# Optimization experiments

Measured on AMD Instinct MI355X. Metric: run time of the kernel, lower is better.

## Reference

```python
import jax, jax.numpy as jnp
import numpy as np

B, S, H = 2, 2048, 1024          # batch, seq, hidden_size
I = 512                          # expert_ffn_hidden_size
E_R, E_Z = 32, 8                 # routed experts, zero (identity) experts
E_T = E_R + E_Z                  # total experts
K = 6                            # moe_topk
SCALE = 2.5                      # routed_scaling_factor
W_INIT = 0.02


def setup_inputs() -> dict:
    key = jax.random.key(0)
    k0, k1, k2, k3 = jax.random.split(key, 4)
    return {
        "hidden_states": jax.random.normal(k0, (B, S, H), jnp.float32),
        "classifier_weight": jax.random.normal(k1, (E_T, H), jnp.float32) * W_INIT,
        "e_score_correction_bias": jnp.zeros((E_T,), jnp.float32),
        "gate_up_proj": jax.random.normal(k2, (E_T, 2 * I, H), jnp.float32) * W_INIT,
        "down_proj": jax.random.normal(k3, (E_R, H, I), jnp.float32) * W_INIT,
    }


def reference(hidden_states, classifier_weight, e_score_correction_bias,
              gate_up_proj, down_proj):
    orig_shape = hidden_states.shape
    x = hidden_states.reshape(-1, H).astype(jnp.float32)      # [T, H]
    T = x.shape[0]

    # ---- router (fp32 like the torch code) ----
    logits = x @ classifier_weight.T                          # [T, E_T]
    scores = jax.nn.softmax(logits, axis=-1)
    _, topk_idx = jax.lax.top_k(scores + e_score_correction_bias[None, :], K)
    topk_w = jnp.take_along_axis(scores, topk_idx, axis=1) * SCALE  # [T, K]

    # dense per-(token, expert) combine weights; 0 for unselected experts
    w_full = jnp.zeros((T, E_T), jnp.float32).at[
        jnp.arange(T)[:, None], topk_idx].add(topk_w)          # [T, E_T]

    # zero experts: weighted identity
    zero_w = w_full[:, E_R:].sum(axis=-1, keepdims=True)       # [T, 1]
    out0 = x * zero_w

    # routed experts: SwiGLU MLP per expert, scanned over experts
    routed_w = w_full[:, :E_R].T                               # [E_R, T]

    def body(out, xs):
        Wgu, Wd, we = xs                                       # [2I,H],[H,I],[T]
        gate, up = jnp.split(x @ Wgu.T, 2, axis=-1)            # [T, I] each
        y = (jax.nn.silu(gate) * up) @ Wd.T                    # [T, H]
        return out + we[:, None] * y, None

    out, _ = jax.lax.scan(body, out0, (gate_up_proj[:E_R], down_proj, routed_w))
    return out.reshape(orig_shape).astype(hidden_states.dtype)
```

## Files before the change

### kernel.cpp

```cpp
#include <hip/hip_runtime.h>
#include <float.h>
#include <math.h>

#define TT 4096
#define HH 1024
#define II 512
#define E_R 32
#define E_T 40
#define TOPK 6
#define SCALE_F 2.5f
#define MAXTILES 224

typedef __bf16 bf16x8 __attribute__((ext_vector_type(8)));
typedef float f32x4 __attribute__((ext_vector_type(4)));

__device__ inline unsigned short f2bf(float f) {
  __bf16 h = (__bf16)f;
  return __builtin_bit_cast(unsigned short, h);
}

__device__ inline bf16x8 cvt8v(float4 a, float4 b) {
  bf16x8 v;
  v[0] = (__bf16)a.x; v[1] = (__bf16)a.y; v[2] = (__bf16)a.z; v[3] = (__bf16)a.w;
  v[4] = (__bf16)b.x; v[5] = (__bf16)b.y; v[6] = (__bf16)b.z; v[7] = (__bf16)b.w;
  return v;
}

__device__ inline void gload_lds16(const void* g, void* l) {
  __builtin_amdgcn_global_load_lds(
      (__attribute__((address_space(1))) void*)g,
      (__attribute__((address_space(3))) void*)l, 16, 0, 0);
}

__device__ inline bf16x8 lds_frag(const unsigned short* base, int row, int kb) {
  int byte = (row * 128 + kb * 2) ^ ((row & 7) << 4);
  uint4 v = *reinterpret_cast<const uint4*>(reinterpret_cast<const char*>(base) + byte);
  return __builtin_bit_cast(bf16x8, v);
}

__device__ inline bf16x8 lds_frag_f32(const float* base, int row, int kb) {
  int key = row & 15;
  int c0 = (kb >> 2) ^ key;
  int c1 = ((kb >> 2) + 1) ^ key;
  const char* p = reinterpret_cast<const char*>(base) + row * 256;
  float4 lo = *reinterpret_cast<const float4*>(p + c0 * 16);
  float4 hi = *reinterpret_cast<const float4*>(p + c1 * 16);
  return cvt8v(lo, hi);
}

__device__ inline f32x4 mfma16(bf16x8 a, bf16x8 b, f32x4 c) {
  return __builtin_amdgcn_mfma_f32_16x16x32_bf16(a, b, c, 0, 0, 0);
}

__global__ __launch_bounds__(256) void k_logits(const float* __restrict__ x,
                                                const float* __restrict__ wcls,
                                                float* __restrict__ logits,
                                                unsigned short* __restrict__ xb,
                                                int* __restrict__ counts) {
  __shared__ float4 ws4[E_T * 64];
  const int tid = threadIdx.x;
  const int lane = tid & 63;
  const int wave = tid >> 6;
  const int token = blockIdx.x * 4 + wave;
  if (blockIdx.x == 0 && tid < E_R) counts[tid] = 0;
  const float4* x4 = reinterpret_cast<const float4*>(x);
  const float4* w4 = reinterpret_cast<const float4*>(wcls);

  float acc[E_T];
  #pragma unroll
  for (int e = 0; e < E_T; ++e) acc[e] = 0.f;

  for (int c = 0; c < 4; ++c) {
    if (c) __syncthreads();
    #pragma unroll
    for (int j = 0; j < 10; ++j) {
      int v = tid + j * 256;
      int e = v >> 6, kq = v & 63;
      ws4[v] = w4[e * 256 + c * 64 + kq];
    }
    float4 xv = x4[(size_t)token * 256 + c * 64 + lane];
    ushort4 s;
    s.x = f2bf(xv.x); s.y = f2bf(xv.y); s.z = f2bf(xv.z); s.w = f2bf(xv.w);
    reinterpret_cast<ushort4*>(xb + (size_t)token * HH)[c * 64 + lane] = s;
    __syncthreads();
    #pragma unroll
    for (int e = 0; e < E_T; ++e) {
      float4 w = ws4[e * 64 + lane];
      acc[e] += xv.x * w.x + xv.y * w.y + xv.z * w.z + xv.w * w.w;
    }
  }

  float mine = 0.f;
  #pragma unroll
  for (int e = 0; e < E_T; ++e) {
    float r = acc[e];
    #pragma unroll
    for (int o = 32; o; o >>= 1) r += __shfl_xor(r, o);
    if (lane == e) mine = r;
  }
  if (lane < E_T) logits[(size_t)token * E_T + lane] = mine;
}

__global__ void k_topk(const float* __restrict__ logits, const float* __restrict__ bias,
                       float* __restrict__ zero_w, int* __restrict__ counts,
                       int* __restrict__ tok_list,
                       int* __restrict__ route_ep, float* __restrict__ route_w,
                       int* __restrict__ route_n) {
  int t = blockIdx.x * 64 + threadIdx.x;
  float l[E_T];
  const float4* lp = reinterpret_cast<const float4*>(logits + (size_t)t * E_T);
  #pragma unroll
  for (int j = 0; j < E_T / 4; ++j) {
    float4 v = lp[j];
    l[j * 4 + 0] = v.x; l[j * 4 + 1] = v.y; l[j * 4 + 2] = v.z; l[j * 4 + 3] = v.w;
  }
  float m = -FLT_MAX;
  #pragma unroll
  for (int e = 0; e < E_T; ++e) m = fmaxf(m, l[e]);
  float den = 0.f;
  #pragma unroll
  for (int e = 0; e < E_T; ++e) { l[e] = __expf(l[e] - m); den += l[e]; }
  float inv = 1.f / den;
  float sel[E_T];
  #pragma unroll
  for (int e = 0; e < E_T; ++e) { l[e] *= inv; sel[e] = l[e] + bias[e]; }

  unsigned long long used = 0ull;
  float zw = 0.f;
  int nr = 0;
  for (int k = 0; k < TOPK; ++k) {
    float bv = -FLT_MAX; int bj = 0;
    #pragma unroll
    for (int e = 0; e < E_T; ++e) {
      float v = ((used >> e) & 1ull) ? -FLT_MAX : sel[e];
      if (v > bv) { bv = v; bj = e; }
    }
    used |= 1ull << bj;
    float wgt = (bv - bias[bj]) * SCALE_F;
    if (bj >= E_R) {
      zw += wgt;
    } else {
      int p = atomicAdd(&counts[bj], 1);
      tok_list[bj * TT + p] = t;
      route_ep[t * TOPK + nr] = (bj << 16) | p;
      route_w[t * TOPK + nr] = wgt;
      nr++;
    }
  }
  zero_w[t] = zw;
  route_n[t] = nr;
}

__global__ void k_scan(const int* __restrict__ counts, int* __restrict__ offsets,
                       int* __restrict__ tiles) {
  if (threadIdx.x == 0) {
    int s = 0, idx = 0;
    for (int e = 0; e < E_R; ++e) {
      offsets[e] = s;
      int c = counts[e];
      s += c;
      for (int r0 = 0; r0 < c; r0 += 128) tiles[1 + idx++] = (e << 16) | r0;
    }
    offsets[E_R] = s;
    tiles[0] = idx;
  }
}

__global__ __launch_bounds__(256, 3) void k_gemm1(
    const unsigned short* __restrict__ xb, const float* __restrict__ gup,
    const int* __restrict__ tok_list, const int* __restrict__ counts,
    const int* __restrict__ offsets, const int* __restrict__ tiles,
    unsigned short* __restrict__ inter) {
  const int nt = tiles[0];
  if ((int)blockIdx.y >= nt) return;
  const int tv = tiles[1 + blockIdx.y];
  const int e = tv >> 16;
  const int row0 = tv & 0xffff;
  const int cnt = counts[e];
  const int off = offsets[e];
  const int n0 = blockIdx.x * 64;
  const int tid = threadIdx.x;
  const int lane = tid & 63;
  const int wave = tid >> 6;
  const int wr = wave >> 1;
  const int wc = wave & 1;

  __shared__ __align__(16) unsigned short lA[128 * 64];
  __shared__ __align__(16) float lBg[64 * 64];
  __shared__ __align__(16) float lBu[64 * 64];
  __shared__ int toks[128];

  if (tid < 128) {
    int r = row0 + tid;
    toks[tid] = tok_list[e * TT + (r < cnt ? r : cnt - 1)];
  }
  __syncthreads();

  unsigned aoff[4];
  #pragma unroll
  for (int i = 0; i < 4; ++i) {
    int lrow = wave * 32 + i * 8 + (lane >> 3);
    aoff[i] = (unsigned)toks[lrow] * HH + (((lane & 7) ^ (lrow & 7)) * 8);
  }
  const float* gbase = gup + (size_t)e * 1024 * HH;
  unsigned boff[4];
  #pragma unroll
  for (int i = 0; i < 4; ++i) {
    int rt = wave * 16 + i * 4 + (lane >> 4);
    boff[i] = (unsigned)(n0 + rt) * HH + (((lane & 15) ^ (rt & 15)) * 4);
  }
  const unsigned upjump = 512u * HH;

  f32x4 accg[4][2] = {}; f32x4 accu[4][2] = {};

  for (int k0 = 0; k0 < HH; k0 += 64) {
    #pragma unroll
    for (int i = 0; i < 4; ++i)
      gload_lds16(xb + aoff[i] + k0, lA + (wave * 32 + i * 8) * 64);
    #pragma unroll
    for (int i = 0; i < 4; ++i) {
      gload_lds16(gbase + boff[i] + k0,          lBg + (wave * 16 + i * 4) * 64);
      gload_lds16(gbase + boff[i] + upjump + k0, lBu + (wave * 16 + i * 4) * 64);
    }
    __syncthreads();
    #pragma unroll
    for (int ks = 0; ks < 2; ++ks) {
      int kb = ks * 32 + ((lane >> 4) << 3);
      bf16x8 a[4], g[2], u[2];
      #pragma unroll
      for (int i = 0; i < 4; ++i) a[i] = lds_frag(lA, wr * 64 + i * 16 + (lane & 15), kb);
      #pragma unroll
      for (int j = 0; j < 2; ++j) {
        g[j] = lds_frag_f32(lBg, wc * 32 + j * 16 + (lane & 15), kb);
        u[j] = lds_frag_f32(lBu, wc * 32 + j * 16 + (lane & 15), kb);
      }
      #pragma unroll
      for (int i = 0; i < 4; ++i)
        #pragma unroll
        for (int j = 0; j < 2; ++j) {
          accg[i][j] = mfma16(a[i], g[j], accg[i][j]);
          accu[i][j] = mfma16(a[i], u[j], accu[i][j]);
        }
    }
    __syncthreads();
  }

  #pragma unroll
  for (int i = 0; i < 4; ++i)
    #pragma unroll
    for (int j = 0; j < 2; ++j)
      #pragma unroll
      for (int r = 0; r < 4; ++r) {
        int rloc = wr * 64 + i * 16 + ((lane >> 4) << 2) + r;
        int grow = row0 + rloc;
        if (grow < cnt) {
          int col = n0 + wc * 32 + j * 16 + (lane & 15);
          float gv = accg[i][j][r], uv = accu[i][j][r];
          float act = gv / (1.f + __expf(-gv)) * uv;
          inter[(size_t)(off + grow) * II + col] = f2bf(act);
        }
      }
}

__global__ __launch_bounds__(256, 3) void k_gemm2(
    const unsigned short* __restrict__ inter, const float* __restrict__ dwn,
    const int* __restrict__ counts, const int* __restrict__ offsets,
    const int* __restrict__ tiles, unsigned short* __restrict__ inter2) {
  const int nt = tiles[0];
  if ((int)blockIdx.y >= nt) return;
  const int tv = tiles[1 + blockIdx.y];
  const int e = tv >> 16;
  const int row0 = tv & 0xffff;
  const int cnt = counts[e];
  const int off = offsets[e];
  const int h0 = blockIdx.x * 128;
  const int tid = threadIdx.x;
  const int lane = tid & 63;
  const int wave = tid >> 6;
  const int wr = wave >> 1;
  const int wc = wave & 1;

  __shared__ __align__(16) unsigned short lA[128 * 64];
  __shared__ __align__(16) float lB[128 * 64];

  unsigned aoff[4];
  #pragma unroll
  for (int i = 0; i < 4; ++i) {
    int lrow = wave * 32 + i * 8 + (lane >> 3);
    int rr = row0 + lrow; rr = rr < cnt ? rr : cnt - 1;
    aoff[i] = (unsigned)(off + rr) * II + (((lane & 7) ^ (lrow & 7)) * 8);
  }
  const float* dbase = dwn + (size_t)e * HH * II;
  unsigned boff[8];
  #pragma unroll
  for (int i = 0; i < 8; ++i) {
    int rt = wave * 32 + i * 4 + (lane >> 4);
    boff[i] = (unsigned)(h0 + rt) * II + (((lane & 15) ^ (rt & 15)) * 4);
  }

  f32x4 acc[4][4] = {};

  for (int k0 = 0; k0 < II; k0 += 64) {
    #pragma unroll
    for (int i = 0; i < 4; ++i)
      gload_lds16(inter + aoff[i] + k0, lA + (wave * 32 + i * 8) * 64);
    #pragma unroll
    for (int i = 0; i < 8; ++i)
      gload_lds16(dbase + boff[i] + k0, lB + (wave * 32 + i * 4) * 64);
    __syncthreads();
    #pragma unroll
    for (int ks = 0; ks < 2; ++ks) {
      int kb = ks * 32 + ((lane >> 4) << 3);
      bf16x8 a[4], b[4];
      #pragma unroll
      for (int i = 0; i < 4; ++i) a[i] = lds_frag(lA, wr * 64 + i * 16 + (lane & 15), kb);
      #pragma unroll
      for (int j = 0; j < 4; ++j) b[j] = lds_frag_f32(lB, wc * 64 + j * 16 + (lane & 15), kb);
      #pragma unroll
      for (int i = 0; i < 4; ++i)
        #pragma unroll
        for (int j = 0; j < 4; ++j)
          acc[i][j] = mfma16(a[i], b[j], acc[i][j]);
    }
    __syncthreads();
  }

  #pragma unroll
  for (int i = 0; i < 4; ++i)
    #pragma unroll
    for (int j = 0; j < 4; ++j)
      #pragma unroll
      for (int r = 0; r < 4; ++r) {
        int rloc = wr * 64 + i * 16 + ((lane >> 4) << 2) + r;
        int grow = row0 + rloc;
        if (grow < cnt) {
          int h = h0 + wc * 64 + j * 16 + (lane & 15);
          inter2[(size_t)(off + grow) * HH + h] = f2bf(acc[i][j][r]);
        }
      }
}

__global__ __launch_bounds__(256) void k_combine(
    const float* __restrict__ x, const float* __restrict__ zero_w,
    const int* __restrict__ offsets, const int* __restrict__ route_ep,
    const float* __restrict__ route_w, const int* __restrict__ route_n,
    const unsigned short* __restrict__ inter2, float* __restrict__ out) {
  const int t = blockIdx.x;
  const int tid = threadIdx.x;
  const float zw = zero_w[t];
  const int n = route_n[t];
  float4 o = reinterpret_cast<const float4*>(x)[t * 256 + tid];
  o.x *= zw; o.y *= zw; o.z *= zw; o.w *= zw;
  for (int i = 0; i < n; ++i) {
    int ep = route_ep[t * TOPK + i];
    int row = offsets[ep >> 16] + (ep & 0xffff);
    float w = route_w[t * TOPK + i];
    ushort4 v = reinterpret_cast<const ushort4*>(inter2 + (size_t)row * HH)[tid];
    o.x += w * __builtin_bit_cast(float, (unsigned)v.x << 16);
    o.y += w * __builtin_bit_cast(float, (unsigned)v.y << 16);
    o.z += w * __builtin_bit_cast(float, (unsigned)v.z << 16);
    o.w += w * __builtin_bit_cast(float, (unsigned)v.w << 16);
  }
  reinterpret_cast<float4*>(out)[t * 256 + tid] = o;
}


extern "C" void kernel_launch(void* const* d_in, const int* in_sizes, int n_in,
                              void* d_out, int out_size, void* d_ws, size_t ws_size,
                              hipStream_t stream) {
  const float* x    = (const float*)d_in[0];
  const float* wcls = (const float*)d_in[1];
  const float* bias = (const float*)d_in[2];
  const float* gup  = (const float*)d_in[3];
  const float* dwn  = (const float*)d_in[4];
  float* out = (float*)d_out;

  char* w = (char*)d_ws;
  unsigned short* xb    = (unsigned short*)(w + 0);
  float* zero_w         = (float*)(w + 8388608);
  int* counts           = (int*)(w + 8404992);
  int* offsets          = (int*)(w + 8405120);
  int* tok_list         = (int*)(w + 8405376);
  float* logits         = (float*)(w + 8929664);
  int* tiles            = (int*)(w + 9585024);
  int* route_ep         = (int*)(w + 9589120);
  float* route_w        = (float*)(w + 9687424);
  int* route_n          = (int*)(w + 9785728);
  unsigned short* inter = (unsigned short*)(w + 9802112);
  unsigned short* inter2 = (unsigned short*)(w + 34967936);

  k_logits<<<1024, 256, 0, stream>>>(x, wcls, logits, xb, counts);
  k_topk<<<64, 64, 0, stream>>>(logits, bias, zero_w, counts, tok_list,
                                route_ep, route_w, route_n);
  k_scan<<<1, 64, 0, stream>>>(counts, offsets, tiles);
  k_gemm1<<<dim3(8, MAXTILES), 256, 0, stream>>>(xb, gup, tok_list, counts, offsets, tiles, inter);
  k_gemm2<<<dim3(8, MAXTILES), 256, 0, stream>>>(inter, dwn, counts, offsets, tiles, inter2);
  k_combine<<<TT, 256, 0, stream>>>(x, zero_w, offsets, route_ep, route_w, route_n,
                                    inter2, out);
}
```

Before: 222.6 us.

## Pre-convert down_proj to bf16 and double-buffer gemm2 LDS loads

```diff
diff --git a/kernel.cpp b/kernel.cpp
--- a/kernel.cpp
+++ b/kernel.cpp
@@ -10,6 +10,7 @@
 #define TOPK 6
 #define SCALE_F 2.5f
 #define MAXTILES 224
+#define NDWN (32*1024*512)
 
 typedef __bf16 bf16x8 __attribute__((ext_vector_type(8)));
 typedef float f32x4 __attribute__((ext_vector_type(4)));
@@ -50,6 +51,19 @@
 
 __device__ inline f32x4 mfma16(bf16x8 a, bf16x8 b, f32x4 c) {
   return __builtin_amdgcn_mfma_f32_16x16x32_bf16(a, b, c, 0, 0, 0);
+}
+
+#define WAIT_VM8()  do { asm volatile("s_waitcnt vmcnt(8)" ::: "memory"); } while (0)
+#define WAIT_VM0()  do { asm volatile("s_waitcnt vmcnt(0)" ::: "memory"); } while (0)
+#define SBAR()      __builtin_amdgcn_s_barrier()
+#define SCHED0()    __builtin_amdgcn_sched_barrier(0)
+
+__global__ __launch_bounds__(256) void k_convert_dwn(const float* __restrict__ dwn,
+                                                     uint4* __restrict__ wb) {
+  unsigned i = blockIdx.x * 256 + threadIdx.x;
+  const float4* src = reinterpret_cast<const float4*>(dwn) + (size_t)i * 2;
+  float4 a = src[0], b = src[1];
+  wb[i] = __builtin_bit_cast(uint4, cvt8v(a, b));
 }
 
 __global__ __launch_bounds__(256) void k_logits(const float* __restrict__ x,
@@ -263,7 +277,7 @@
 }
 
 __global__ __launch_bounds__(256, 3) void k_gemm2(
-    const unsigned short* __restrict__ inter, const float* __restrict__ dwn,
+    const unsigned short* __restrict__ inter, const unsigned short* __restrict__ dwnb,
     const int* __restrict__ counts, const int* __restrict__ offsets,
     const int* __restrict__ tiles, unsigned short* __restrict__ inter2) {
   const int nt = tiles[0];
@@ -280,8 +294,8 @@
   const int wr = wave >> 1;
   const int wc = wave & 1;
 
-  __shared__ __align__(16) unsigned short lA[128 * 64];
-  __shared__ __align__(16) float lB[128 * 64];
+  __shared__ __align__(16) unsigned short lA[2][128 * 64];
+  __shared__ __align__(16) unsigned short lB[2][128 * 64];
 
   unsigned aoff[4];
   #pragma unroll
@@ -290,40 +304,65 @@
     int rr = row0 + lrow; rr = rr < cnt ? rr : cnt - 1;
     aoff[i] = (unsigned)(off + rr) * II + (((lane & 7) ^ (lrow & 7)) * 8);
   }
-  const float* dbase = dwn + (size_t)e * HH * II;
-  unsigned boff[8];
-  #pragma unroll
-  for (int i = 0; i < 8; ++i) {
-    int rt = wave * 32 + i * 4 + (lane >> 4);
-    boff[i] = (unsigned)(h0 + rt) * II + (((lane & 15) ^ (rt & 15)) * 4);
+  const unsigned short* db = dwnb + (size_t)e * (HH * II);
+  unsigned boff[4];
+  #pragma unroll
+  for (int i = 0; i < 4; ++i) {
+    int lrow = wave * 32 + i * 8 + (lane >> 3);
+    boff[i] = (unsigned)(h0 + lrow) * II + (((lane & 7) ^ (lrow & 7)) * 8);
   }
 
   f32x4 acc[4][4] = {};
 
-  for (int k0 = 0; k0 < II; k0 += 64) {
-    #pragma unroll
-    for (int i = 0; i < 4; ++i)
-      gload_lds16(inter + aoff[i] + k0, lA + (wave * 32 + i * 8) * 64);
-    #pragma unroll
-    for (int i = 0; i < 8; ++i)
-      gload_lds16(dbase + boff[i] + k0, lB + (wave * 32 + i * 4) * 64);
-    __syncthreads();
-    #pragma unroll
-    for (int ks = 0; ks < 2; ++ks) {
-      int kb = ks * 32 + ((lane >> 4) << 3);
-      bf16x8 a[4], b[4];
-      #pragma unroll
-      for (int i = 0; i < 4; ++i) a[i] = lds_frag(lA, wr * 64 + i * 16 + (lane & 15), kb);
-      #pragma unroll
-      for (int j = 0; j < 4; ++j) b[j] = lds_frag_f32(lB, wc * 64 + j * 16 + (lane & 15), kb);
-      #pragma unroll
-      for (int i = 0; i < 4; ++i)
-        #pragma unroll
-        for (int j = 0; j < 4; ++j)
-          acc[i][j] = mfma16(a[i], b[j], acc[i][j]);
-    }
-    __syncthreads();
-  }
+#define G2_STAGE(T, B)                                                          \
+  {                                                                             \
+    int k0s = (T) * 64;                                                         \
+    _Pragma("unroll")                                                           \
+    for (int i = 0; i < 4; ++i)                                                 \
+      gload_lds16(inter + aoff[i] + k0s, lA[B] + (wave * 32 + i * 8) * 64);     \
+    _Pragma("unroll")                                                           \
+    for (int i = 0; i < 4; ++i)                                                 \
+      gload_lds16(db + boff[i] + k0s, lB[B] + (wave * 32 + i * 8) * 64);        \
+  }
+
+#define G2_COMPUTE(B)                                                           \
+  {                                                                             \
+    _Pragma("unroll")                                                           \
+    for (int ks = 0; ks < 2; ++ks) {                                            \
+      int kb = ks * 32 + ((lane >> 4) << 3);                                    \
+      bf16x8 a[4], b[4];                                                        \
+      _Pragma("unroll")                                                         \
+      for (int i = 0; i < 4; ++i) a[i] = lds_frag(lA[B], wr * 64 + i * 16 + (lane & 15), kb); \
+      _Pragma("unroll")                                                         \
+      for (int j = 0; j < 4; ++j) b[j] = lds_frag(lB[B], wc * 64 + j * 16 + (lane & 15), kb); \
+      _Pragma("unroll")                                                         \
+      for (int i = 0; i < 4; ++i)                                               \
+        _Pragma("unroll")                                                       \
+        for (int j = 0; j < 4; ++j)                                             \
+          acc[i][j] = mfma16(a[i], b[j], acc[i][j]);                            \
+    }                                                                           \
+  }
+
+  G2_STAGE(0, 0);
+  G2_STAGE(1, 1);
+  WAIT_VM8();
+  SBAR(); SCHED0();
+
+  #pragma unroll 2
+  for (int t = 0; t < 6; ++t) {
+    if (t & 1) { G2_COMPUTE(1); } else { G2_COMPUTE(0); }
+    SCHED0();
+    SBAR();
+    if (t & 1) { G2_STAGE(t + 2, 1); } else { G2_STAGE(t + 2, 0); }
+    WAIT_VM8();
+    SBAR(); SCHED0();
+  }
+  G2_COMPUTE(0);
+  SCHED0();
+  SBAR();
+  WAIT_VM0();
+  SBAR(); SCHED0();
+  G2_COMPUTE(1);
 
   #pragma unroll
   for (int i = 0; i < 4; ++i)
@@ -388,13 +427,15 @@
   int* route_n          = (int*)(w + 9785728);
   unsigned short* inter = (unsigned short*)(w + 9802112);
   unsigned short* inter2 = (unsigned short*)(w + 34967936);
-
+  unsigned short* dwnb  = (unsigned short*)(w + 85299584);
+
+  k_convert_dwn<<<NDWN / 8 / 256, 256, 0, stream>>>(dwn, (uint4*)dwnb);
   k_logits<<<1024, 256, 0, stream>>>(x, wcls, logits, xb, counts);
   k_topk<<<64, 64, 0, stream>>>(logits, bias, zero_w, counts, tok_list,
                                 route_ep, route_w, route_n);
   k_scan<<<1, 64, 0, stream>>>(counts, offsets, tiles);
   k_gemm1<<<dim3(8, MAXTILES), 256, 0, stream>>>(xb, gup, tok_list, counts, offsets, tiles, inter);
-  k_gemm2<<<dim3(8, MAXTILES), 256, 0, stream>>>(inter, dwn, counts, offsets, tiles, inter2);
+  k_gemm2<<<dim3(8, MAXTILES), 256, 0, stream>>>(inter, dwnb, counts, offsets, tiles, inter2);
   k_combine<<<TT, 256, 0, stream>>>(x, zero_w, offsets, route_ep, route_w, route_n,
                                     inter2, out);
 }
```

After: 236.9 us. +6.4%, slower.

## Fold scan into topk via last-block ticket and remap GEMM grid for XCD locality

Applied to the files above, without the earlier changes.

```diff
diff --git a/kernel.cpp b/kernel.cpp
--- a/kernel.cpp
+++ b/kernel.cpp
@@ -56,13 +56,17 @@
                                                 const float* __restrict__ wcls,
                                                 float* __restrict__ logits,
                                                 unsigned short* __restrict__ xb,
-                                                int* __restrict__ counts) {
+                                                int* __restrict__ counts,
+                                                int* __restrict__ ticket) {
   __shared__ float4 ws4[E_T * 64];
   const int tid = threadIdx.x;
   const int lane = tid & 63;
   const int wave = tid >> 6;
   const int token = blockIdx.x * 4 + wave;
-  if (blockIdx.x == 0 && tid < E_R) counts[tid] = 0;
+  if (blockIdx.x == 0) {
+    if (tid < E_R) counts[tid] = 0;
+    else if (tid == E_R) *ticket = 0;
+  }
   const float4* x4 = reinterpret_cast<const float4*>(x);
   const float4* w4 = reinterpret_cast<const float4*>(wcls);
 
@@ -105,7 +109,9 @@
                        float* __restrict__ zero_w, int* __restrict__ counts,
                        int* __restrict__ tok_list,
                        int* __restrict__ route_ep, float* __restrict__ route_w,
-                       int* __restrict__ route_n) {
+                       int* __restrict__ route_n,
+                       int* __restrict__ offsets, int* __restrict__ tiles,
+                       int* __restrict__ ticket) {
   int t = blockIdx.x * 64 + threadIdx.x;
   float l[E_T];
   const float4* lp = reinterpret_cast<const float4*>(logits + (size_t)t * E_T);
@@ -149,20 +155,22 @@
   }
   zero_w[t] = zw;
   route_n[t] = nr;
-}
-
-__global__ void k_scan(const int* __restrict__ counts, int* __restrict__ offsets,
-                       int* __restrict__ tiles) {
+
+  __threadfence();
+  __syncthreads();
   if (threadIdx.x == 0) {
-    int s = 0, idx = 0;
-    for (int e = 0; e < E_R; ++e) {
-      offsets[e] = s;
-      int c = counts[e];
-      s += c;
-      for (int r0 = 0; r0 < c; r0 += 128) tiles[1 + idx++] = (e << 16) | r0;
-    }
-    offsets[E_R] = s;
-    tiles[0] = idx;
+    int tk = atomicAdd(ticket, 1);
+    if (tk == (int)gridDim.x - 1) {
+      int s = 0, idx = 0;
+      for (int e = 0; e < E_R; ++e) {
+        int c = atomicAdd(&counts[e], 0);
+        offsets[e] = s;
+        s += c;
+        for (int r0 = 0; r0 < c; r0 += 128) tiles[1 + idx++] = (e << 16) | r0;
+      }
+      offsets[E_R] = s;
+      tiles[0] = idx;
+    }
   }
 }
 
@@ -171,14 +179,17 @@
     const int* __restrict__ tok_list, const int* __restrict__ counts,
     const int* __restrict__ offsets, const int* __restrict__ tiles,
     unsigned short* __restrict__ inter) {
+  const int fid = blockIdx.x;
+  const int w = (fid & 7) * MAXTILES + (fid >> 3);
+  const int ty = w >> 3;
   const int nt = tiles[0];
-  if ((int)blockIdx.y >= nt) return;
-  const int tv = tiles[1 + blockIdx.y];
+  if (ty >= nt) return;
+  const int tv = tiles[1 + ty];
   const int e = tv >> 16;
   const int row0 = tv & 0xffff;
   const int cnt = counts[e];
   const int off = offsets[e];
-  const int n0 = blockIdx.x * 64;
+  const int n0 = (w & 7) * 64;
   const int tid = threadIdx.x;
   const int lane = tid & 63;
   const int wave = tid >> 6;
@@ -266,14 +277,17 @@
     const unsigned short* __restrict__ inter, const float* __restrict__ dwn,
     const int* __restrict__ counts, const int* __restrict__ offsets,
     const int* __restrict__ tiles, unsigned short* __restrict__ inter2) {
+  const int fid = blockIdx.x;
+  const int w = (fid & 7) * MAXTILES + (fid >> 3);
+  const int ty = w >> 3;
   const int nt = tiles[0];
-  if ((int)blockIdx.y >= nt) return;
-  const int tv = tiles[1 + blockIdx.y];
+  if (ty >= nt) return;
+  const int tv = tiles[1 + ty];
   const int e = tv >> 16;
   const int row0 = tv & 0xffff;
   const int cnt = counts[e];
   const int off = offsets[e];
-  const int h0 = blockIdx.x * 128;
+  const int h0 = (w & 7) * 128;
   const int tid = threadIdx.x;
   const int lane = tid & 63;
   const int wave = tid >> 6;
@@ -380,6 +394,7 @@
   float* zero_w         = (float*)(w + 8388608);
   int* counts           = (int*)(w + 8404992);
   int* offsets          = (int*)(w + 8405120);
+  int* ticket           = (int*)(w + 8405120 + 160);
   int* tok_list         = (int*)(w + 8405376);
   float* logits         = (float*)(w + 8929664);
   int* tiles            = (int*)(w + 9585024);
@@ -389,12 +404,11 @@
   unsigned short* inter = (unsigned short*)(w + 9802112);
   unsigned short* inter2 = (unsigned short*)(w + 34967936);
 
-  k_logits<<<1024, 256, 0, stream>>>(x, wcls, logits, xb, counts);
+  k_logits<<<1024, 256, 0, stream>>>(x, wcls, logits, xb, counts, ticket);
   k_topk<<<64, 64, 0, stream>>>(logits, bias, zero_w, counts, tok_list,
-                                route_ep, route_w, route_n);
-  k_scan<<<1, 64, 0, stream>>>(counts, offsets, tiles);
-  k_gemm1<<<dim3(8, MAXTILES), 256, 0, stream>>>(xb, gup, tok_list, counts, offsets, tiles, inter);
-  k_gemm2<<<dim3(8, MAXTILES), 256, 0, stream>>>(inter, dwn, counts, offsets, tiles, inter2);
+                                route_ep, route_w, route_n, offsets, tiles, ticket);
+  k_gemm1<<<dim3(8 * MAXTILES), 256, 0, stream>>>(xb, gup, tok_list, counts, offsets, tiles, inter);
+  k_gemm2<<<dim3(8 * MAXTILES), 256, 0, stream>>>(inter, dwn, counts, offsets, tiles, inter2);
   k_combine<<<TT, 256, 0, stream>>>(x, zero_w, offsets, route_ep, route_w, route_n,
                                     inter2, out);
 }
```

After: 247.6 us. 1.11x slower.

## Fuse combine into down-proj epilogue via atomics and merge scan into top-k

Applied to the files above, without the earlier changes.

```diff
diff --git a/kernel.cpp b/kernel.cpp
--- a/kernel.cpp
+++ b/kernel.cpp
@@ -56,13 +56,17 @@
                                                 const float* __restrict__ wcls,
                                                 float* __restrict__ logits,
                                                 unsigned short* __restrict__ xb,
-                                                int* __restrict__ counts) {
+                                                int* __restrict__ counts,
+                                                int* __restrict__ ticket) {
   __shared__ float4 ws4[E_T * 64];
   const int tid = threadIdx.x;
   const int lane = tid & 63;
   const int wave = tid >> 6;
   const int token = blockIdx.x * 4 + wave;
-  if (blockIdx.x == 0 && tid < E_R) counts[tid] = 0;
+  if (blockIdx.x == 0) {
+    if (tid < E_R) counts[tid] = 0;
+    else if (tid == E_R) *ticket = 0;
+  }
   const float4* x4 = reinterpret_cast<const float4*>(x);
   const float4* w4 = reinterpret_cast<const float4*>(wcls);
 
@@ -101,68 +105,83 @@
   if (lane < E_T) logits[(size_t)token * E_T + lane] = mine;
 }
 
-__global__ void k_topk(const float* __restrict__ logits, const float* __restrict__ bias,
-                       float* __restrict__ zero_w, int* __restrict__ counts,
-                       int* __restrict__ tok_list,
-                       int* __restrict__ route_ep, float* __restrict__ route_w,
-                       int* __restrict__ route_n) {
-  int t = blockIdx.x * 64 + threadIdx.x;
-  float l[E_T];
-  const float4* lp = reinterpret_cast<const float4*>(logits + (size_t)t * E_T);
-  #pragma unroll
-  for (int j = 0; j < E_T / 4; ++j) {
-    float4 v = lp[j];
-    l[j * 4 + 0] = v.x; l[j * 4 + 1] = v.y; l[j * 4 + 2] = v.z; l[j * 4 + 3] = v.w;
-  }
-  float m = -FLT_MAX;
-  #pragma unroll
-  for (int e = 0; e < E_T; ++e) m = fmaxf(m, l[e]);
-  float den = 0.f;
-  #pragma unroll
-  for (int e = 0; e < E_T; ++e) { l[e] = __expf(l[e] - m); den += l[e]; }
-  float inv = 1.f / den;
-  float sel[E_T];
-  #pragma unroll
-  for (int e = 0; e < E_T; ++e) { l[e] *= inv; sel[e] = l[e] + bias[e]; }
-
-  unsigned long long used = 0ull;
-  float zw = 0.f;
-  int nr = 0;
-  for (int k = 0; k < TOPK; ++k) {
-    float bv = -FLT_MAX; int bj = 0;
-    #pragma unroll
-    for (int e = 0; e < E_T; ++e) {
-      float v = ((used >> e) & 1ull) ? -FLT_MAX : sel[e];
-      if (v > bv) { bv = v; bj = e; }
-    }
-    used |= 1ull << bj;
-    float wgt = (bv - bias[bj]) * SCALE_F;
-    if (bj >= E_R) {
-      zw += wgt;
-    } else {
-      int p = atomicAdd(&counts[bj], 1);
-      tok_list[bj * TT + p] = t;
-      route_ep[t * TOPK + nr] = (bj << 16) | p;
-      route_w[t * TOPK + nr] = wgt;
-      nr++;
-    }
-  }
-  zero_w[t] = zw;
-  route_n[t] = nr;
-}
-
-__global__ void k_scan(const int* __restrict__ counts, int* __restrict__ offsets,
-                       int* __restrict__ tiles) {
-  if (threadIdx.x == 0) {
-    int s = 0, idx = 0;
-    for (int e = 0; e < E_R; ++e) {
-      offsets[e] = s;
-      int c = counts[e];
-      s += c;
-      for (int r0 = 0; r0 < c; r0 += 128) tiles[1 + idx++] = (e << 16) | r0;
-    }
-    offsets[E_R] = s;
-    tiles[0] = idx;
+__global__ __launch_bounds__(256) void k_topk(
+    const float* __restrict__ logits, const float* __restrict__ bias,
+    const float* __restrict__ x, int* __restrict__ counts,
+    int* __restrict__ tok_list, float* __restrict__ wt_list,
+    float* __restrict__ out,
+    int* __restrict__ offsets, int* __restrict__ tiles, int* __restrict__ ticket) {
+  __shared__ float s_zw[64];
+  const int tid = threadIdx.x;
+  if (tid < 64) {
+    int t = blockIdx.x * 64 + tid;
+    float l[E_T];
+    const float4* lp = reinterpret_cast<const float4*>(logits + (size_t)t * E_T);
+    #pragma unroll
+    for (int j = 0; j < E_T / 4; ++j) {
+      float4 v = lp[j];
+      l[j * 4 + 0] = v.x; l[j * 4 + 1] = v.y; l[j * 4 + 2] = v.z; l[j * 4 + 3] = v.w;
+    }
+    float m = -FLT_MAX;
+    #pragma unroll
+    for (int e = 0; e < E_T; ++e) m = fmaxf(m, l[e]);
+    float den = 0.f;
+    #pragma unroll
+    for (int e = 0; e < E_T; ++e) { l[e] = __expf(l[e] - m); den += l[e]; }
+    float inv = 1.f / den;
+    float sel[E_T];
+    #pragma unroll
+    for (int e = 0; e < E_T; ++e) { l[e] *= inv; sel[e] = l[e] + bias[e]; }
+
+    unsigned long long used = 0ull;
+    float zw = 0.f;
+    for (int k = 0; k < TOPK; ++k) {
+      float bv = -FLT_MAX; int bj = 0;
+      #pragma unroll
+      for (int e = 0; e < E_T; ++e) {
+        float v = ((used >> e) & 1ull) ? -FLT_MAX : sel[e];
+        if (v > bv) { bv = v; bj = e; }
+      }
+      used |= 1ull << bj;
+      float wgt = (bv - bias[bj]) * SCALE_F;
+      if (bj >= E_R) {
+        zw += wgt;
+      } else {
+        int p = atomicAdd(&counts[bj], 1);
+        tok_list[bj * TT + p] = t;
+        wt_list[bj * TT + p] = wgt;
+      }
+    }
+    s_zw[tid] = zw;
+  }
+  __syncthreads();
+
+  const float4* x4 = reinterpret_cast<const float4*>(x) + (size_t)blockIdx.x * 64 * 256;
+  float4* o4 = reinterpret_cast<float4*>(out) + (size_t)blockIdx.x * 64 * 256;
+  #pragma unroll
+  for (int j = 0; j < 64; ++j) {
+    int i = tid + j * 256;
+    float zw = s_zw[i >> 8];
+    float4 v = x4[i];
+    v.x *= zw; v.y *= zw; v.z *= zw; v.w *= zw;
+    o4[i] = v;
+  }
+
+  __threadfence();
+  __syncthreads();
+  if (tid == 0) {
+    int tk = atomicAdd(ticket, 1);
+    if (tk == (int)gridDim.x - 1) {
+      int s = 0, idx = 0;
+      for (int e = 0; e < E_R; ++e) {
+        int c = atomicAdd(&counts[e], 0);
+        offsets[e] = s;
+        s += c;
+        for (int r0 = 0; r0 < c; r0 += 128) tiles[1 + idx++] = (e << 16) | r0;
+      }
+      offsets[E_R] = s;
+      tiles[0] = idx;
+    }
   }
 }
 
@@ -264,8 +283,9 @@
 
 __global__ __launch_bounds__(256, 3) void k_gemm2(
     const unsigned short* __restrict__ inter, const float* __restrict__ dwn,
+    const int* __restrict__ tok_list, const float* __restrict__ wt_list,
     const int* __restrict__ counts, const int* __restrict__ offsets,
-    const int* __restrict__ tiles, unsigned short* __restrict__ inter2) {
+    const int* __restrict__ tiles, float* __restrict__ out) {
   const int nt = tiles[0];
   if ((int)blockIdx.y >= nt) return;
   const int tv = tiles[1 + blockIdx.y];
@@ -282,6 +302,16 @@
 
   __shared__ __align__(16) unsigned short lA[128 * 64];
   __shared__ __align__(16) float lB[128 * 64];
+  __shared__ int toks[128];
+  __shared__ float wts[128];
+
+  if (tid < 128) {
+    int r = row0 + tid;
+    int rc = r < cnt ? r : cnt - 1;
+    toks[tid] = tok_list[e * TT + rc];
+    wts[tid] = (r < cnt) ? wt_list[e * TT + rc] : 0.f;
+  }
+  __syncthreads();
 
   unsigned aoff[4];
   #pragma unroll
@@ -335,33 +365,9 @@
         int grow = row0 + rloc;
         if (grow < cnt) {
           int h = h0 + wc * 64 + j * 16 + (lane & 15);
-          inter2[(size_t)(off + grow) * HH + h] = f2bf(acc[i][j][r]);
+          unsafeAtomicAdd(&out[(size_t)toks[rloc] * HH + h], acc[i][j][r] * wts[rloc]);
         }
       }
-}
-
-__global__ __launch_bounds__(256) void k_combine(
-    const float* __restrict__ x, const float* __restrict__ zero_w,
-    const int* __restrict__ offsets, const int* __restrict__ route_ep,
-    const float* __restrict__ route_w, const int* __restrict__ route_n,
-    const unsigned short* __restrict__ inter2, float* __restrict__ out) {
-  const int t = blockIdx.x;
-  const int tid = threadIdx.x;
-  const float zw = zero_w[t];
-  const int n = route_n[t];
-  float4 o = reinterpret_cast<const float4*>(x)[t * 256 + tid];
-  o.x *= zw; o.y *= zw; o.z *= zw; o.w *= zw;
-  for (int i = 0; i < n; ++i) {
-    int ep = route_ep[t * TOPK + i];
-    int row = offsets[ep >> 16] + (ep & 0xffff);
-    float w = route_w[t * TOPK + i];
-    ushort4 v = reinterpret_cast<const ushort4*>(inter2 + (size_t)row * HH)[tid];
-    o.x += w * __builtin_bit_cast(float, (unsigned)v.x << 16);
-    o.y += w * __builtin_bit_cast(float, (unsigned)v.y << 16);
-    o.z += w * __builtin_bit_cast(float, (unsigned)v.z << 16);
-    o.w += w * __builtin_bit_cast(float, (unsigned)v.w << 16);
-  }
-  reinterpret_cast<float4*>(out)[t * 256 + tid] = o;
 }
 
 
@@ -377,24 +383,19 @@
 
   char* w = (char*)d_ws;
   unsigned short* xb    = (unsigned short*)(w + 0);
-  float* zero_w         = (float*)(w + 8388608);
-  int* counts           = (int*)(w + 8404992);
-  int* offsets          = (int*)(w + 8405120);
-  int* tok_list         = (int*)(w + 8405376);
-  float* logits         = (float*)(w + 8929664);
-  int* tiles            = (int*)(w + 9585024);
-  int* route_ep         = (int*)(w + 9589120);
-  float* route_w        = (float*)(w + 9687424);
-  int* route_n          = (int*)(w + 9785728);
-  unsigned short* inter = (unsigned short*)(w + 9802112);
-  unsigned short* inter2 = (unsigned short*)(w + 34967936);
-
-  k_logits<<<1024, 256, 0, stream>>>(x, wcls, logits, xb, counts);
-  k_topk<<<64, 64, 0, stream>>>(logits, bias, zero_w, counts, tok_list,
-                                route_ep, route_w, route_n);
-  k_scan<<<1, 64, 0, stream>>>(counts, offsets, tiles);
+  int* counts           = (int*)(w + 8388608);
+  int* offsets          = (int*)(w + 8388736);
+  int* ticket           = (int*)(w + 8388736 + 160);
+  int* tok_list         = (int*)(w + 8388992);
+  float* wt_list        = (float*)(w + 8913280);
+  float* logits         = (float*)(w + 9437568);
+  int* tiles            = (int*)(w + 10092928);
+  unsigned short* inter = (unsigned short*)(w + 10097024);
+
+  k_logits<<<1024, 256, 0, stream>>>(x, wcls, logits, xb, counts, ticket);
+  k_topk<<<64, 256, 0, stream>>>(logits, bias, x, counts, tok_list, wt_list,
+                                 out, offsets, tiles, ticket);
   k_gemm1<<<dim3(8, MAXTILES), 256, 0, stream>>>(xb, gup, tok_list, counts, offsets, tiles, inter);
-  k_gemm2<<<dim3(8, MAXTILES), 256, 0, stream>>>(inter, dwn, counts, offsets, tiles, inter2);
-  k_combine<<<TT, 256, 0, stream>>>(x, zero_w, offsets, route_ep, route_w, route_n,
-                                    inter2, out);
-}
+  k_gemm2<<<dim3(8, MAXTILES), 256, 0, stream>>>(inter, dwn, tok_list, wt_list, counts,
+                                                 offsets, tiles, out);
+}
```

After: 259.1 us. +16.4%, slower.
